# Kernel optimization log

Hardware: AMD Instinct MI355X
Metric: run time of the kernel (lower is better)

Reference implementation:

```python
import jax, jax.numpy as jnp
import numpy as np

B, T, N_IN, N_RES, N_OUT = 64, 512, 2000, 50, 500
SPECTRAL_RADIUS = 0.7


def setup_inputs() -> dict:
    key = jax.random.key(0)
    k_x, k_in, k_res, k_ker, k_b = jax.random.split(key, 5)
    inputs = jax.random.normal(k_x, (B, T, N_IN), dtype=jnp.float32)
    W_in = jax.random.uniform(k_in, (N_RES, N_IN), minval=-0.5, maxval=0.5, dtype=jnp.float32)
    W_res_raw = np.asarray(jax.random.uniform(k_res, (N_RES, N_RES), minval=-0.5, maxval=0.5, dtype=jnp.float32))
    # spectral-radius normalization (host-side eig, matches tf.linalg.eigvals scaling)
    rho = np.max(np.abs(np.linalg.eigvals(W_res_raw.astype(np.float64))))
    W_res = jnp.asarray((W_res_raw / rho * SPECTRAL_RADIUS).astype(np.float32))
    # Dense(n_outputs, tanh): glorot-uniform kernel, zero bias
    lim = np.sqrt(6.0 / (N_RES + N_OUT))
    W_out_kernel = jax.random.uniform(k_ker, (N_RES, N_OUT), minval=-lim, maxval=lim, dtype=jnp.float32)
    W_out_bias = jnp.zeros((N_OUT,), dtype=jnp.float32)
    return {"inputs": inputs, "W_in": W_in, "W_res": W_res,
            "W_out_kernel": W_out_kernel, "W_out_bias": W_out_bias}


def reference(inputs, W_in, W_res, W_out_kernel, W_out_bias):
    # inputs: [B, T, n_in]; recurrence: state = tanh(tanh(u) @ W_in^T + state @ W_res^T)
    batch = inputs.shape[0]
    state0 = jnp.zeros((batch, W_in.shape[0]), dtype=inputs.dtype)

    def step(state, u_t):  # u_t: [B, n_in]
        u = jnp.tanh(u_t)
        new_state = jnp.tanh(u @ W_in.T + state @ W_res.T)
        return new_state, None

    final_state, _ = jax.lax.scan(step, state0, jnp.swapaxes(inputs, 0, 1))
    # readout uses only the last state: Dense(tanh)
    return jnp.tanh(final_state @ W_out_kernel + W_out_bias)
```

## Files before the change

kernel.cpp:

```cpp
#include <hip/hip_runtime.h>
#include <cstdint>

#define NIN     2000
#define NRES    50
#define NOUT    500
#define TSTEPS  512
#define NBATCH  64
#define BT      32768
#define KSTEPS  63
#define SPAD    64
#define KCLAMP  1996

typedef __bf16 bf16x8 __attribute__((ext_vector_type(8)));
typedef float  f32x4  __attribute__((ext_vector_type(4)));

__device__ __forceinline__ float fast_tanh(float x) {
  float e = __expf(2.0f * x);
  return fmaf(-2.0f, __builtin_amdgcn_rcpf(e + 1.0f), 1.0f);
}

__device__ __forceinline__ void bf16_split(float x, unsigned short& h, unsigned short& l) {
  unsigned u  = __float_as_uint(x);
  unsigned hb = (u + 0x7FFFu + ((u >> 16) & 1u)) & 0xFFFF0000u;
  h = (unsigned short)(hb >> 16);
  float lo = x - __uint_as_float(hb);
  l = (unsigned short)(__float_as_uint(lo) >> 16);
}

union ABfrag { unsigned short u16[8]; bf16x8 v; };

__global__ __launch_bounds__(256) void prep_kernel(const float* __restrict__ Win,
                                                   unsigned short* __restrict__ Bpk) {
  int tid  = blockIdx.x * 256 + threadIdx.x;
  int l    = tid & 63;
  int rest = tid >> 6;
  int f    = rest & 3;
  int p    = (rest >> 2) & 1;
  int s    = rest >> 3;
  int n    = f * 16 + (l & 15);
  int kb   = s * 32 + (l >> 4) * 8;
  unsigned short v[8];
#pragma unroll
  for (int j = 0; j < 8; ++j) {
    int k = kb + j;
    float x = (n < NRES && k < NIN) ? Win[n * NIN + k] : 0.0f;
    unsigned short h, lo;
    bf16_split(x, h, lo);
    v[j] = p ? lo : h;
  }
  *reinterpret_cast<uint4*>(Bpk + (size_t)tid * 8) = *reinterpret_cast<uint4*>(v);
}

__global__ __launch_bounds__(256, 2) void proj_mfma(const float* __restrict__ U,
                                                    const unsigned short* __restrict__ Bpk,
                                                    float* __restrict__ P) {
  __shared__ __align__(16) unsigned short lds[2][4096];
  const int wave = threadIdx.x >> 6;
  const int lane = threadIdx.x & 63;
  const int mrow = lane & 15;
  const int g    = lane >> 4;
  const int g8   = g * 8;
  const int row0 = (blockIdx.x * 4 + wave) * 16;

  const float* __restrict__ u = U + (size_t)(row0 + mrow) * NIN;

  const int c0 = wave * 2, c1 = c0 + 1;
  const unsigned short* src0 = Bpk + ((size_t)c0 * 64 + lane) * 8;
  const unsigned short* src1 = Bpk + ((size_t)c1 * 64 + lane) * 8;
  unsigned short* dst0[2] = { &lds[0][(c0 * 64 + lane) * 8], &lds[1][(c0 * 64 + lane) * 8] };
  unsigned short* dst1[2] = { &lds[0][(c1 * 64 + lane) * 8], &lds[1][(c1 * 64 + lane) * 8] };

  f32x4 acc[4] = {};

  {
    uint4 s0 = *reinterpret_cast<const uint4*>(src0);
    uint4 s1 = *reinterpret_cast<const uint4*>(src1);
    *reinterpret_cast<uint4*>(dst0[0]) = s0;
    *reinterpret_cast<uint4*>(dst1[0]) = s1;
  }
  float4 ca = *(const float4*)(u + min(g8, KCLAMP));
  float4 cb = *(const float4*)(u + min(g8 + 4, KCLAMP));
  __syncthreads();

  for (int s = 0; s < KSTEPS; ++s) {
    const int cur = s & 1, nxt = cur ^ 1;
    const int kn = s * 32 + 32;

    uint4 n0 = *reinterpret_cast<const uint4*>(src0 + (size_t)(s + 1) * 4096);
    uint4 n1 = *reinterpret_cast<const uint4*>(src1 + (size_t)(s + 1) * 4096);
    float4 na = *(const float4*)(u + min(kn + g8, KCLAMP));
    float4 nb = *(const float4*)(u + min(kn + g8 + 4, KCLAMP));

    bf16x8 bh[4], bl[4];
#pragma unroll
    for (int f = 0; f < 4; ++f) {
      bh[f] = *(const bf16x8*)&lds[cur][(f * 64 + lane) * 8];
      bl[f] = *(const bf16x8*)&lds[cur][((4 + f) * 64 + lane) * 8];
    }

    float t[8];
    t[0] = fast_tanh(ca.x); t[1] = fast_tanh(ca.y);
    t[2] = fast_tanh(ca.z); t[3] = fast_tanh(ca.w);
    t[4] = fast_tanh(cb.x); t[5] = fast_tanh(cb.y);
    t[6] = fast_tanh(cb.z); t[7] = fast_tanh(cb.w);

    ABfrag ah, al;
#pragma unroll
    for (int j = 0; j < 8; ++j) bf16_split(t[j], ah.u16[j], al.u16[j]);

#pragma unroll
    for (int f = 0; f < 4; ++f)
      acc[f] = __builtin_amdgcn_mfma_f32_16x16x32_bf16(ah.v, bh[f], acc[f], 0, 0, 0);
#pragma unroll
    for (int f = 0; f < 4; ++f)
      acc[f] = __builtin_amdgcn_mfma_f32_16x16x32_bf16(al.v, bh[f], acc[f], 0, 0, 0);
#pragma unroll
    for (int f = 0; f < 4; ++f)
      acc[f] = __builtin_amdgcn_mfma_f32_16x16x32_bf16(ah.v, bl[f], acc[f], 0, 0, 0);

    *reinterpret_cast<uint4*>(dst0[nxt]) = n0;
    *reinterpret_cast<uint4*>(dst1[nxt]) = n1;
    __syncthreads();

    ca = na; cb = nb;
  }

#pragma unroll
  for (int f = 0; f < 4; ++f) {
    const int col = f * 16 + mrow;
    if (col < NRES) {
#pragma unroll
      for (int i = 0; i < 4; ++i) {
        const int r = row0 + g * 4 + i;
        P[(size_t)r * NRES + col] = acc[f][i];
      }
    }
  }
}

__global__ __launch_bounds__(64, 1) void recur_kernel(const float* __restrict__ P,
                                                      const float* __restrict__ W_res,
                                                      const float* __restrict__ W_out,
                                                      const float* __restrict__ bias,
                                                      float* __restrict__ out) {
  __shared__ float sbuf[64];
  const int b    = blockIdx.x;
  const int lane = threadIdx.x;
  const int r    = (lane < NRES) ? lane : 0;

  float w[52];
#pragma unroll
  for (int j = 0; j < NRES; ++j) w[j] = W_res[r * NRES + j];
  w[50] = 0.0f; w[51] = 0.0f;

  const float* Pb = P + (size_t)b * TSTEPS * NRES;
  float state = 0.0f;

  float pring[16];
#pragma unroll
  for (int i = 0; i < 16; ++i) pring[i] = Pb[i * NRES + r];

#pragma unroll 16
  for (int t = 0; t < TSTEPS; ++t) {
    float pcur = pring[t & 15];
    pring[t & 15] = Pb[(t + 16) * NRES + r];

    sbuf[lane] = state;
    __builtin_amdgcn_wave_barrier();

    float a0 = pcur, a1 = 0.0f, a2 = 0.0f, a3 = 0.0f;
    float a4 = 0.0f, a5 = 0.0f, a6 = 0.0f, a7 = 0.0f;
#pragma unroll
    for (int q = 0; q < 12; q += 2) {
      float4 sA = *(const float4*)&sbuf[q * 4];
      float4 sB = *(const float4*)&sbuf[q * 4 + 4];
      a0 = fmaf(sA.x, w[4 * q + 0], a0);
      a1 = fmaf(sA.y, w[4 * q + 1], a1);
      a2 = fmaf(sA.z, w[4 * q + 2], a2);
      a3 = fmaf(sA.w, w[4 * q + 3], a3);
      a4 = fmaf(sB.x, w[4 * q + 4], a4);
      a5 = fmaf(sB.y, w[4 * q + 5], a5);
      a6 = fmaf(sB.z, w[4 * q + 6], a6);
      a7 = fmaf(sB.w, w[4 * q + 7], a7);
    }
    {
      float4 sA = *(const float4*)&sbuf[48];
      a0 = fmaf(sA.x, w[48], a0);
      a1 = fmaf(sA.y, w[49], a1);
      a2 = fmaf(sA.z, w[50], a2);
      a3 = fmaf(sA.w, w[51], a3);
    }
    state = fast_tanh(((a0 + a1) + (a2 + a3)) + ((a4 + a5) + (a6 + a7)));
  }

  sbuf[lane] = state;
  __builtin_amdgcn_wave_barrier();

#pragma unroll
  for (int kk = 0; kk < 8; ++kk) {
    int o = kk * 64 + lane;
    if (o < NOUT) {
      float a0 = bias[o];
      float a1 = 0.0f;
#pragma unroll
      for (int q = 0; q < 12; ++q) {
        float4 s4 = *(const float4*)&sbuf[q * 4];
        a0 = fmaf(s4.x, W_out[(4 * q + 0) * NOUT + o], a0);
        a1 = fmaf(s4.y, W_out[(4 * q + 1) * NOUT + o], a1);
        a0 = fmaf(s4.z, W_out[(4 * q + 2) * NOUT + o], a0);
        a1 = fmaf(s4.w, W_out[(4 * q + 3) * NOUT + o], a1);
      }
      {
        float4 s4 = *(const float4*)&sbuf[48];
        a0 = fmaf(s4.x, W_out[48 * NOUT + o], a0);
        a1 = fmaf(s4.y, W_out[49 * NOUT + o], a1);
      }
      out[b * NOUT + o] = fast_tanh(a0 + a1);
    }
  }
}

extern "C" void kernel_launch(void* const* d_in, const int* in_sizes, int n_in,
                              void* d_out, int out_size, void* d_ws, size_t ws_size,
                              hipStream_t stream) {
  const float* inputs = (const float*)d_in[0];
  const float* W_in   = (const float*)d_in[1];
  const float* W_res  = (const float*)d_in[2];
  const float* W_out  = (const float*)d_in[3];
  const float* bias   = (const float*)d_in[4];
  float* out = (float*)d_out;

  float* P = (float*)d_ws;
  unsigned short* Bpk = (unsigned short*)((char*)d_ws + (size_t)BT * NRES * 4);

  prep_kernel<<<128, 256, 0, stream>>>(W_in, Bpk);
  proj_mfma<<<BT / 64, 256, 0, stream>>>(inputs, Bpk, P);
  recur_kernel<<<NBATCH, 64, 0, stream>>>(P, W_res, W_out, bias, out);
}
```

Measured before the change: 569.8 us.

## Cooperatively stage tanh'd A tiles in LDS and use readlane broadcast in recurrence

The projection kernel now loads the input rows cooperatively (four threads per row, each handling eight K values), computes tanh and the bf16 hi/lo split once, and writes the A fragments into double-buffered LDS one stage ahead. The MFMA loop then reads A fragments from LDS alongside the B fragments. This overlaps the transcendental work with the matrix ops and changes the global read pattern, at the cost of more LDS traffic. In the recurrence kernel, the per-step LDS store/load of the state is replaced by readlane broadcasts into the FMAs, shortening the serial dependency chain each timestep.

Measured after the change: 483.3 us. -15.2%, faster.

```diff
diff --git a/kernel.cpp b/kernel.cpp
--- a/kernel.cpp
+++ b/kernel.cpp
@@ -8,8 +8,6 @@
 #define NBATCH  64
 #define BT      32768
 #define KSTEPS  63
-#define SPAD    64
-#define KCLAMP  1996
 
 typedef __bf16 bf16x8 __attribute__((ext_vector_type(8)));
 typedef float  f32x4  __attribute__((ext_vector_type(4)));
@@ -54,72 +52,87 @@
 __global__ __launch_bounds__(256, 2) void proj_mfma(const float* __restrict__ U,
                                                     const unsigned short* __restrict__ Bpk,
                                                     float* __restrict__ P) {
-  __shared__ __align__(16) unsigned short lds[2][4096];
-  const int wave = threadIdx.x >> 6;
-  const int lane = threadIdx.x & 63;
+  __shared__ __align__(16) unsigned short ldsA[2][2][2048];
+  __shared__ __align__(16) unsigned short ldsB[2][4096];
+
+  const int tid  = threadIdx.x;
+  const int wave = tid >> 6;
+  const int lane = tid & 63;
   const int mrow = lane & 15;
   const int g    = lane >> 4;
-  const int g8   = g * 8;
-  const int row0 = (blockIdx.x * 4 + wave) * 16;
-
-  const float* __restrict__ u = U + (size_t)(row0 + mrow) * NIN;
+  const int row0 = blockIdx.x * 64 + wave * 16;
+
+  const int rw   = tid >> 2;
+  const int koct = tid & 3;
+  const float* __restrict__ urow = U + (size_t)(blockIdx.x * 64 + rw) * NIN;
+  const int kfix  = koct * 8;
+  const int aslot = (rw >> 4) * 512 + ((koct << 4) | (rw & 15)) * 8;
 
   const int c0 = wave * 2, c1 = c0 + 1;
-  const unsigned short* src0 = Bpk + ((size_t)c0 * 64 + lane) * 8;
-  const unsigned short* src1 = Bpk + ((size_t)c1 * 64 + lane) * 8;
-  unsigned short* dst0[2] = { &lds[0][(c0 * 64 + lane) * 8], &lds[1][(c0 * 64 + lane) * 8] };
-  unsigned short* dst1[2] = { &lds[0][(c1 * 64 + lane) * 8], &lds[1][(c1 * 64 + lane) * 8] };
+  const unsigned short* srcB0 = Bpk + ((size_t)c0 * 64 + lane) * 8;
+  const unsigned short* srcB1 = Bpk + ((size_t)c1 * 64 + lane) * 8;
+  const int bslot0 = (c0 * 64 + lane) * 8;
+  const int bslot1 = (c1 * 64 + lane) * 8;
 
   f32x4 acc[4] = {};
 
+  auto stageA = [&](int st, float4 a0, float4 a1) {
+    float t[8];
+    t[0] = fast_tanh(a0.x); t[1] = fast_tanh(a0.y);
+    t[2] = fast_tanh(a0.z); t[3] = fast_tanh(a0.w);
+    t[4] = fast_tanh(a1.x); t[5] = fast_tanh(a1.y);
+    t[6] = fast_tanh(a1.z); t[7] = fast_tanh(a1.w);
+    ABfrag h, l;
+#pragma unroll
+    for (int j = 0; j < 8; ++j) bf16_split(t[j], h.u16[j], l.u16[j]);
+    *reinterpret_cast<bf16x8*>(&ldsA[st][0][aslot]) = h.v;
+    *reinterpret_cast<bf16x8*>(&ldsA[st][1][aslot]) = l.v;
+  };
+
   {
-    uint4 s0 = *reinterpret_cast<const uint4*>(src0);
-    uint4 s1 = *reinterpret_cast<const uint4*>(src1);
-    *reinterpret_cast<uint4*>(dst0[0]) = s0;
-    *reinterpret_cast<uint4*>(dst1[0]) = s1;
-  }
-  float4 ca = *(const float4*)(u + min(g8, KCLAMP));
-  float4 cb = *(const float4*)(u + min(g8 + 4, KCLAMP));
+    float4 a0 = *(const float4*)(urow + kfix);
+    float4 a1 = *(const float4*)(urow + kfix + 4);
+    uint4  b0 = *(const uint4*)(srcB0);
+    uint4  b1 = *(const uint4*)(srcB1);
+    stageA(0, a0, a1);
+    *reinterpret_cast<uint4*>(&ldsB[0][bslot0]) = b0;
+    *reinterpret_cast<uint4*>(&ldsB[0][bslot1]) = b1;
+  }
+  float4 ca = *(const float4*)(urow + 32 + kfix);
+  float4 cb = *(const float4*)(urow + 32 + kfix + 4);
   __syncthreads();
 
   for (int s = 0; s < KSTEPS; ++s) {
     const int cur = s & 1, nxt = cur ^ 1;
-    const int kn = s * 32 + 32;
-
-    uint4 n0 = *reinterpret_cast<const uint4*>(src0 + (size_t)(s + 1) * 4096);
-    uint4 n1 = *reinterpret_cast<const uint4*>(src1 + (size_t)(s + 1) * 4096);
-    float4 na = *(const float4*)(u + min(kn + g8, KCLAMP));
-    float4 nb = *(const float4*)(u + min(kn + g8 + 4, KCLAMP));
-
+
+    const int kb = (s + 2) * 32 + kfix;
+    float4 na = *(const float4*)(urow + min(kb, 1992));
+    float4 nb = *(const float4*)(urow + min(kb + 4, 1996));
+    uint4  n0 = *(const uint4*)(srcB0 + (size_t)(s + 1) * 4096);
+    uint4  n1 = *(const uint4*)(srcB1 + (size_t)(s + 1) * 4096);
+
+    bf16x8 ah = *(const bf16x8*)&ldsA[cur][0][wave * 512 + lane * 8];
+    bf16x8 al = *(const bf16x8*)&ldsA[cur][1][wave * 512 + lane * 8];
     bf16x8 bh[4], bl[4];
 #pragma unroll
     for (int f = 0; f < 4; ++f) {
-      bh[f] = *(const bf16x8*)&lds[cur][(f * 64 + lane) * 8];
-      bl[f] = *(const bf16x8*)&lds[cur][((4 + f) * 64 + lane) * 8];
-    }
-
-    float t[8];
-    t[0] = fast_tanh(ca.x); t[1] = fast_tanh(ca.y);
-    t[2] = fast_tanh(ca.z); t[3] = fast_tanh(ca.w);
-    t[4] = fast_tanh(cb.x); t[5] = fast_tanh(cb.y);
-    t[6] = fast_tanh(cb.z); t[7] = fast_tanh(cb.w);
-
-    ABfrag ah, al;
-#pragma unroll
-    for (int j = 0; j < 8; ++j) bf16_split(t[j], ah.u16[j], al.u16[j]);
+      bh[f] = *(const bf16x8*)&ldsB[cur][(f * 64 + lane) * 8];
+      bl[f] = *(const bf16x8*)&ldsB[cur][((4 + f) * 64 + lane) * 8];
+    }
 
 #pragma unroll
     for (int f = 0; f < 4; ++f)
-      acc[f] = __builtin_amdgcn_mfma_f32_16x16x32_bf16(ah.v, bh[f], acc[f], 0, 0, 0);
+      acc[f] = __builtin_amdgcn_mfma_f32_16x16x32_bf16(ah, bh[f], acc[f], 0, 0, 0);
 #pragma unroll
     for (int f = 0; f < 4; ++f)
-      acc[f] = __builtin_amdgcn_mfma_f32_16x16x32_bf16(al.v, bh[f], acc[f], 0, 0, 0);
+      acc[f] = __builtin_amdgcn_mfma_f32_16x16x32_bf16(al, bh[f], acc[f], 0, 0, 0);
 #pragma unroll
     for (int f = 0; f < 4; ++f)
-      acc[f] = __builtin_amdgcn_mfma_f32_16x16x32_bf16(ah.v, bl[f], acc[f], 0, 0, 0);
-
-    *reinterpret_cast<uint4*>(dst0[nxt]) = n0;
-    *reinterpret_cast<uint4*>(dst1[nxt]) = n1;
+      acc[f] = __builtin_amdgcn_mfma_f32_16x16x32_bf16(ah, bl[f], acc[f], 0, 0, 0);
+
+    stageA(nxt, ca, cb);
+    *reinterpret_cast<uint4*>(&ldsB[nxt][bslot0]) = n0;
+    *reinterpret_cast<uint4*>(&ldsB[nxt][bslot1]) = n1;
     __syncthreads();
 
     ca = na; cb = nb;
@@ -136,6 +149,10 @@
       }
     }
   }
+}
+
+__device__ __forceinline__ float rl(float v, int j) {
+  return __uint_as_float(__builtin_amdgcn_readlane(__float_as_uint(v), j));
 }
 
 __global__ __launch_bounds__(64, 1) void recur_kernel(const float* __restrict__ P,
@@ -148,10 +165,9 @@
   const int lane = threadIdx.x;
   const int r    = (lane < NRES) ? lane : 0;
 
-  float w[52];
+  float w[NRES];
 #pragma unroll
   for (int j = 0; j < NRES; ++j) w[j] = W_res[r * NRES + j];
-  w[50] = 0.0f; w[51] = 0.0f;
 
   const float* Pb = P + (size_t)b * TSTEPS * NRES;
   float state = 0.0f;
@@ -165,36 +181,26 @@
     float pcur = pring[t & 15];
     pring[t & 15] = Pb[(t + 16) * NRES + r];
 
-    sbuf[lane] = state;
-    __builtin_amdgcn_wave_barrier();
-
     float a0 = pcur, a1 = 0.0f, a2 = 0.0f, a3 = 0.0f;
     float a4 = 0.0f, a5 = 0.0f, a6 = 0.0f, a7 = 0.0f;
 #pragma unroll
-    for (int q = 0; q < 12; q += 2) {
-      float4 sA = *(const float4*)&sbuf[q * 4];
-      float4 sB = *(const float4*)&sbuf[q * 4 + 4];
-      a0 = fmaf(sA.x, w[4 * q + 0], a0);
-      a1 = fmaf(sA.y, w[4 * q + 1], a1);
-      a2 = fmaf(sA.z, w[4 * q + 2], a2);
-      a3 = fmaf(sA.w, w[4 * q + 3], a3);
-      a4 = fmaf(sB.x, w[4 * q + 4], a4);
-      a5 = fmaf(sB.y, w[4 * q + 5], a5);
-      a6 = fmaf(sB.z, w[4 * q + 6], a6);
-      a7 = fmaf(sB.w, w[4 * q + 7], a7);
-    }
-    {
-      float4 sA = *(const float4*)&sbuf[48];
-      a0 = fmaf(sA.x, w[48], a0);
-      a1 = fmaf(sA.y, w[49], a1);
-      a2 = fmaf(sA.z, w[50], a2);
-      a3 = fmaf(sA.w, w[51], a3);
-    }
+    for (int j = 0; j < 48; j += 8) {
+      a0 = fmaf(rl(state, j + 0), w[j + 0], a0);
+      a1 = fmaf(rl(state, j + 1), w[j + 1], a1);
+      a2 = fmaf(rl(state, j + 2), w[j + 2], a2);
+      a3 = fmaf(rl(state, j + 3), w[j + 3], a3);
+      a4 = fmaf(rl(state, j + 4), w[j + 4], a4);
+      a5 = fmaf(rl(state, j + 5), w[j + 5], a5);
+      a6 = fmaf(rl(state, j + 6), w[j + 6], a6);
+      a7 = fmaf(rl(state, j + 7), w[j + 7], a7);
+    }
+    a0 = fmaf(rl(state, 48), w[48], a0);
+    a1 = fmaf(rl(state, 49), w[49], a1);
     state = fast_tanh(((a0 + a1) + (a2 + a3)) + ((a4 + a5) + (a6 + a7)));
   }
 
   sbuf[lane] = state;
-  __builtin_amdgcn_wave_barrier();
+  __syncthreads();
 
 #pragma unroll
   for (int kk = 0; kk < 8; ++kk) {
```
